# Kernel optimization log

Hardware: AMD Instinct MI355X
Metric: run time of the kernel (lower is better)

Reference implementation:

```python
import jax, jax.numpy as jnp
import numpy as np

N_NODES = 500_000
N_EDGES = 4_000_000


def setup_inputs() -> dict:
    key = jax.random.key(0)
    k1, k2, k3, k4 = jax.random.split(key, 4)
    x = jax.random.normal(k1, (N_NODES, 3), dtype=jnp.float32)
    edge_index = jax.random.randint(k2, (2, N_EDGES), 0, N_NODES, dtype=jnp.int32)
    # GCNConv(3, 16) and GCNConv(16, 1): weight [in, out], bias [out]
    W1 = jax.random.normal(k3, (3, 16), dtype=jnp.float32) / np.sqrt(3.0)
    b1 = jnp.zeros((16,), dtype=jnp.float32)
    W2 = jax.random.normal(k4, (16, 1), dtype=jnp.float32) / np.sqrt(16.0)
    b2 = jnp.zeros((1,), dtype=jnp.float32)
    return {"x": x, "edge_index": edge_index, "W1": W1, "b1": b1, "W2": W2, "b2": b2}


def gcn_conv(x, edge_index, W, b):
    """PyG GCNConv: add self-loops, symmetric deg^-1/2 normalization,
    linear transform, scatter-add aggregation to target nodes, bias."""
    n = x.shape[0]
    loop = jnp.arange(n, dtype=edge_index.dtype)
    row = jnp.concatenate([edge_index[0], loop])  # source nodes
    col = jnp.concatenate([edge_index[1], loop])  # target nodes
    deg = jax.ops.segment_sum(jnp.ones_like(col, dtype=x.dtype), col, num_segments=n)
    deg_inv_sqrt = jnp.where(deg > 0, jax.lax.rsqrt(jnp.maximum(deg, 1.0)), 0.0)
    norm = deg_inv_sqrt[row] * deg_inv_sqrt[col]  # [E+N]
    h = x @ W  # [N, out]
    msg = h[row] * norm[:, None]  # gather + scale, [E+N, out]
    out = jax.ops.segment_sum(msg, col, num_segments=n)  # scatter-add
    return out + b


def reference(x, edge_index, W1, b1, W2, b2):
    h = jax.nn.relu(gcn_conv(x, edge_index, W1, b1))
    return gcn_conv(h, edge_index, W2, b2)  # [N, 1]
```

## Files before the change

kernel.cpp:

```cpp
#include <hip/hip_runtime.h>
#include <hip/hip_fp16.h>


typedef float vf4 __attribute__((ext_vector_type(4)));

#define NB 512
#define SHIFT 10
#define SLICE 1024
#define CAP 11264
#define P1T 1024
#define P1PER 16
#define P1G 256
#define SENT 0xFFFFFFFFu

__global__ __launch_bounds__(1024) void p1_partition(
        const int* __restrict__ row, const int* __restrict__ col,
        unsigned* __restrict__ gcur, unsigned* __restrict__ buf, int E) {
    __shared__ unsigned hist[NB];
    __shared__ unsigned loff[NB], lcur[NB], gbase[NB];
    __shared__ unsigned stage[P1T * P1PER];
    __shared__ unsigned wsum[16];
    int t = threadIdx.x;
    if (t < NB) hist[t] = 0;
    __syncthreads();
    int per = (E + P1G - 1) / P1G;
    per = (per + 3) & ~3;
    long long base = (long long)blockIdx.x * per;
    long long eend = base + per; if (eend > E) eend = E;
    int nch = (per + 4095) / 4096;
    unsigned ent[P1PER];
    int bkt[P1PER];
#pragma unroll
    for (int ch = 0; ch < 4; ch++) {
        if (ch < nch) {
            long long e = base + (long long)ch * 4096 + 4 * t;
            if (e + 3 < eend) {
                int4 c4 = *(const int4*)(col + e);
                int4 r4 = *(const int4*)(row + e);
                int cs[4] = {c4.x, c4.y, c4.z, c4.w};
                int rs[4] = {r4.x, r4.y, r4.z, r4.w};
#pragma unroll
                for (int u = 0; u < 4; u++) {
                    int j = ch * 4 + u;
                    ent[j] = ((unsigned)rs[u] << SHIFT) | (unsigned)(cs[u] & (SLICE - 1));
                    bkt[j] = cs[u] >> SHIFT;
                    atomicAdd(&hist[bkt[j]], 1u);
                }
            } else {
#pragma unroll
                for (int u = 0; u < 4; u++) {
                    int j = ch * 4 + u;
                    long long ee = e + u;
                    if (ee < eend) {
                        int c = col[ee], r = row[ee];
                        ent[j] = ((unsigned)r << SHIFT) | (unsigned)(c & (SLICE - 1));
                        bkt[j] = c >> SHIFT;
                        atomicAdd(&hist[bkt[j]], 1u);
                    } else bkt[j] = -1;
                }
            }
        } else {
#pragma unroll
            for (int u = 0; u < 4; u++) bkt[ch * 4 + u] = -1;
        }
    }
    __syncthreads();
    unsigned myc = 0, v = 0;
    int lane = t & 63, w = t >> 6;
    if (t < NB) {
        myc = hist[t];
        v = myc;
#pragma unroll
        for (int d = 1; d < 64; d <<= 1) {
            unsigned o = __shfl_up(v, d, 64);
            if (lane >= d) v += o;
        }
        if (lane == 63) wsum[w] = v;
    }
    __syncthreads();
    if (w == 0) {
        unsigned s = (lane < 8) ? wsum[lane] : 0u, sv = s;
#pragma unroll
        for (int d = 1; d < 8; d <<= 1) {
            unsigned o = __shfl_up(sv, d, 64);
            if (lane >= d) sv += o;
        }
        if (lane < 8) wsum[lane] = sv - s;
    }
    __syncthreads();
    if (t < NB) {
        unsigned excl = v - myc + wsum[w];
        loff[t] = excl;
        lcur[t] = excl;
        unsigned padded = (myc + 15u) & ~15u;
        gbase[t] = padded ? atomicAdd(&gcur[t], padded) : 0u;
        hist[t] = padded;
    }
    __syncthreads();
#pragma unroll
    for (int j = 0; j < P1PER; j++) {
        if (bkt[j] >= 0) {
            unsigned p = atomicAdd(&lcur[bkt[j]], 1u);
            stage[p] = ent[j];
        }
    }
    __syncthreads();
    if (t < NB) {
        unsigned c = myc, padded = hist[t], lo = loff[t], gb = gbase[t];
        unsigned* dst = buf + (size_t)t * CAP + gb;
        for (unsigned s = 0; s + 4 <= padded && gb + s + 4 <= CAP; s += 4) {
            uint4 q;
            q.x = (s + 0 < c) ? stage[lo + s + 0] : SENT;
            q.y = (s + 1 < c) ? stage[lo + s + 1] : SENT;
            q.z = (s + 2 < c) ? stage[lo + s + 2] : SENT;
            q.w = (s + 3 < c) ? stage[lo + s + 3] : SENT;
            *(uint4*)(dst + s) = q;
        }
    }
}

__global__ __launch_bounds__(1024) void k2a1(
        const unsigned* __restrict__ gcur, const unsigned* __restrict__ buf,
        const float* __restrict__ x, uint2* __restrict__ xs4h,
        unsigned* __restrict__ pstart, int N) {
    __shared__ unsigned cnts[SLICE];
    __shared__ unsigned wsum[16];
    int b = blockIdx.x, t = threadIdx.x;
    cnts[t] = 0;
    __syncthreads();
    unsigned ext = min(gcur[b], (unsigned)CAP);
    const unsigned* bp = buf + (size_t)b * CAP;
    for (unsigned i = 4 * t; i < ext; i += 4096) {
        uint4 q = *(const uint4*)(bp + i);
        if (q.x != SENT) atomicAdd(&cnts[q.x & (SLICE - 1)], 1u);
        if (q.y != SENT) atomicAdd(&cnts[q.y & (SLICE - 1)], 1u);
        if (q.z != SENT) atomicAdd(&cnts[q.z & (SLICE - 1)], 1u);
        if (q.w != SENT) atomicAdd(&cnts[q.w & (SLICE - 1)], 1u);
    }
    __syncthreads();
    unsigned myc = cnts[t];
    unsigned pc = (myc + 3u) & ~3u;
    unsigned v = pc;
    int lane = t & 63, w = t >> 6;
#pragma unroll
    for (int d = 1; d < 64; d <<= 1) {
        unsigned o = __shfl_up(v, d, 64);
        if (lane >= d) v += o;
    }
    if (lane == 63) wsum[w] = v;
    __syncthreads();
    if (w == 0) {
        unsigned s = (lane < 16) ? wsum[lane] : 0u, sv = s;
#pragma unroll
        for (int d = 1; d < 16; d <<= 1) {
            unsigned o = __shfl_up(sv, d, 64);
            if (lane >= d) sv += o;
        }
        if (lane < 16) wsum[lane] = sv - s;
    }
    __syncthreads();
    unsigned excl = v - pc + wsum[w];
    int c = (b << SHIFT) + t;
    pstart[c] = (excl << 8) | min(myc, 255u);
    if (c < N) {
        float d = rsqrtf(1.0f + (float)myc);
        __half2 h01 = __floats2half2_rn(d * x[3 * c], d * x[3 * c + 1]);
        __half2 h23 = __floats2half2_rn(d * x[3 * c + 2], 0.f);
        uint2 u;
        u.x = *(unsigned*)&h01;
        u.y = *(unsigned*)&h23;
        xs4h[c] = u;
    }
}

__global__ __launch_bounds__(1024) void k2bf(
        const unsigned* __restrict__ gcur, const unsigned* __restrict__ buf,
        const unsigned* __restrict__ pstart, const uint2* __restrict__ xs4h,
        const float* __restrict__ W1, const float* __restrict__ b1,
        const float* __restrict__ W2, unsigned* __restrict__ buf2,
        float* __restrict__ hs2, int N) {
    __shared__ __align__(16) unsigned sorted[CAP];
    __shared__ unsigned pos[SLICE];
    __shared__ unsigned stot;
    __shared__ float sW[48], sb[16], sw2[16];
    int b = blockIdx.x, t = threadIdx.x;
    if (t < 48) sW[t] = W1[t];
    if (t < 16) { sb[t] = b1[t]; sw2[t] = W2[t]; }
    unsigned meta = pstart[(b << SHIFT) + t];
    pos[t] = meta >> 8;
    if (t == SLICE - 1) {
        unsigned tt = (meta >> 8) + (((meta & 255u) + 3u) & ~3u);
        stot = min(tt, (unsigned)CAP);
    }
    __syncthreads();
    unsigned ext = min(gcur[b], (unsigned)CAP);
    const unsigned* bp = buf + (size_t)b * CAP;
    for (unsigned i = 4 * t; i < ext; i += 4096) {
        uint4 q = *(const uint4*)(bp + i);
        if (q.x != SENT) { unsigned p = atomicAdd(&pos[q.x & (SLICE - 1)], 1u); if (p < CAP) sorted[p] = q.x >> SHIFT; }
        if (q.y != SENT) { unsigned p = atomicAdd(&pos[q.y & (SLICE - 1)], 1u); if (p < CAP) sorted[p] = q.y >> SHIFT; }
        if (q.z != SENT) { unsigned p = atomicAdd(&pos[q.z & (SLICE - 1)], 1u); if (p < CAP) sorted[p] = q.z >> SHIFT; }
        if (q.w != SENT) { unsigned p = atomicAdd(&pos[q.w & (SLICE - 1)], 1u); if (p < CAP) sorted[p] = q.w >> SHIFT; }
    }
    __syncthreads();
    unsigned tot = stot;
    unsigned* b2p = buf2 + (size_t)b * CAP;
    for (unsigned i = 4 * t; i < tot; i += 4096)
        *(uint4*)(b2p + i) = *(const uint4*)(sorted + i);
    int c = (b << SHIFT) + t;
    if (c >= N) return;
    unsigned cnt = meta & 255u;
    unsigned base = meta >> 8;
    float d = rsqrtf(1.0f + (float)cnt);
    uint2 us = xs4h[c];
    float2 fs = __half22float2(*(__half2*)&us.x);
    float a0 = fs.x, a1 = fs.y, a2 = __low2float(*(__half2*)&us.y);
    unsigned j = 0;
    for (; j + 4 <= cnt; j += 4) {
        uint4 rr = *(const uint4*)(sorted + base + j);
        uint2 u0 = xs4h[rr.x], u1 = xs4h[rr.y], u2 = xs4h[rr.z], u3 = xs4h[rr.w];
        float2 f0 = __half22float2(*(__half2*)&u0.x); float g0 = __low2float(*(__half2*)&u0.y);
        float2 f1 = __half22float2(*(__half2*)&u1.x); float g1 = __low2float(*(__half2*)&u1.y);
        float2 f2 = __half22float2(*(__half2*)&u2.x); float g2 = __low2float(*(__half2*)&u2.y);
        float2 f3 = __half22float2(*(__half2*)&u3.x); float g3 = __low2float(*(__half2*)&u3.y);
        a0 += (f0.x + f1.x) + (f2.x + f3.x);
        a1 += (f0.y + f1.y) + (f2.y + f3.y);
        a2 += (g0 + g1) + (g2 + g3);
    }
    for (; j < cnt; j++) {
        uint2 u = xs4h[sorted[base + j]];
        float2 f = __half22float2(*(__half2*)&u.x);
        a0 += f.x; a1 += f.y; a2 += __low2float(*(__half2*)&u.y);
    }
    float s = 0.f;
#pragma unroll
    for (int k = 0; k < 16; k++) {
        float z = fmaxf(d * (a0 * sW[k] + a1 * sW[16 + k] + a2 * sW[32 + k]) + sb[k], 0.f);
        s += z * sw2[k];
    }
    hs2[c] = d * s;
}

__global__ __launch_bounds__(1024) void k2c(
        const unsigned* __restrict__ pstart, const unsigned* __restrict__ buf2,
        const float* __restrict__ hs2, const float* __restrict__ b2,
        float* __restrict__ out, int N) {
    int b = blockIdx.x, t = threadIdx.x;
    int c = (b << SHIFT) + t;
    if (c >= N) return;
    unsigned meta = pstart[c];
    const unsigned* sp = buf2 + (size_t)b * CAP + (meta >> 8);
    unsigned cnt = meta & 255u;
    float d = rsqrtf(1.0f + (float)cnt);
    float s = hs2[c];
    unsigned j = 0;
    for (; j + 4 <= cnt; j += 4) {
        uint4 rr = *(const uint4*)(sp + j);
        float v0 = hs2[rr.x], v1 = hs2[rr.y], v2 = hs2[rr.z], v3 = hs2[rr.w];
        s += (v0 + v1) + (v2 + v3);
    }
    for (; j < cnt; j++) s += hs2[sp[j]];
    out[c] = d * s + b2[0];
}

__global__ void fb_deg(const int* __restrict__ col, float* __restrict__ deg, int E) {
    int e = blockIdx.x * blockDim.x + threadIdx.x;
    if (e < E) atomicAdd(&deg[col[e]], 1.0f);
}
__global__ void fb_pass_a(const float* __restrict__ x, const float* __restrict__ deg,
                          float* __restrict__ dis, vf4* __restrict__ xs4, int N) {
    int i = blockIdx.x * blockDim.x + threadIdx.x;
    if (i >= N) return;
    float d = rsqrtf(deg[i] + 1.0f);
    dis[i] = d;
    vf4 v; v.x = d * x[3 * i]; v.y = d * x[3 * i + 1]; v.z = d * x[3 * i + 2]; v.w = 0.f;
    xs4[i] = v;
}
__global__ void fb_aggx(const int* __restrict__ ei, const float* __restrict__ xs4,
                        float* __restrict__ accx, int E) {
    int t = blockIdx.x * blockDim.x + threadIdx.x;
    int e = t >> 2, k = t & 3;
    if (e >= E) return;
    int r = ei[e], c = ei[E + e];
    float val = xs4[4 * r + k];
    if (k < 3) atomicAdd(&accx[4 * c + k], val);
}
__global__ void fb_post1(const vf4* __restrict__ accx, const vf4* __restrict__ xs4,
                         const float* __restrict__ dis, const float* __restrict__ W1,
                         const float* __restrict__ b1, const float* __restrict__ W2,
                         float* __restrict__ hs2, int N) {
    __shared__ float sW[48], sb[16], sw2[16];
    if (threadIdx.x < 48) sW[threadIdx.x] = W1[threadIdx.x];
    if (threadIdx.x < 16) { sb[threadIdx.x] = b1[threadIdx.x]; sw2[threadIdx.x] = W2[threadIdx.x]; }
    __syncthreads();
    int i = blockIdx.x * blockDim.x + threadIdx.x;
    if (i >= N) return;
    vf4 a = accx[i], self = xs4[i];
    float a0 = a.x + self.x, a1 = a.y + self.y, a2 = a.z + self.z;
    float d = dis[i], s = 0.f;
#pragma unroll
    for (int k = 0; k < 16; k++) {
        float z = fmaxf(d * (a0 * sW[k] + a1 * sW[16 + k] + a2 * sW[32 + k]) + sb[k], 0.f);
        s += z * sw2[k];
    }
    hs2[i] = d * s;
}
__global__ void fb_agg2(const int* __restrict__ ei, const float* __restrict__ hs2,
                        float* __restrict__ acc2, int E) {
    int e = blockIdx.x * blockDim.x + threadIdx.x;
    if (e >= E) return;
    atomicAdd(&acc2[ei[E + e]], hs2[ei[e]]);
}
__global__ void fb_fin(const float* __restrict__ acc2, const float* __restrict__ hs2,
                       const float* __restrict__ dis, const float* __restrict__ b2,
                       float* __restrict__ out, int N) {
    int i = blockIdx.x * blockDim.x + threadIdx.x;
    if (i < N) out[i] = dis[i] * (acc2[i] + hs2[i]) + b2[0];
}

extern "C" void kernel_launch(void* const* d_in, const int* in_sizes, int n_in,
                              void* d_out, int out_size, void* d_ws, size_t ws_size,
                              hipStream_t stream) {
    const float* x  = (const float*)d_in[0];
    const int*   ei = (const int*)d_in[1];
    const float* W1 = (const float*)d_in[2];
    const float* b1 = (const float*)d_in[3];
    const float* W2 = (const float*)d_in[4];
    const float* b2 = (const float*)d_in[5];
    float* out = (float*)d_out;

    const int N = in_sizes[0] / 3;
    const int E = in_sizes[1] / 2;
    const int* row = ei;
    const int* col = ei + E;

    float* ws = (float*)d_ws;
    size_t need = (size_t)(1024 + 2 * (size_t)NB * CAP + 3 * (size_t)N
                           + (size_t)NB * SLICE) * 4;

    if (ws_size >= need) {
        unsigned* gcur = (unsigned*)ws;
        unsigned* buf  = (unsigned*)ws + 1024;
        unsigned* buf2 = buf + (size_t)NB * CAP;
        uint2* xs4h = (uint2*)(buf2 + (size_t)NB * CAP);
        float* hs2  = (float*)(xs4h + N);
        unsigned* pstart = (unsigned*)(hs2 + N);

        hipMemsetAsync(gcur, 0, 1024 * sizeof(unsigned), stream);
        p1_partition<<<P1G, P1T, 0, stream>>>(row, col, gcur, buf, E);
        k2a1<<<NB, 1024, 0, stream>>>(gcur, buf, x, xs4h, pstart, N);
        k2bf<<<NB, 1024, 0, stream>>>(gcur, buf, pstart, xs4h, W1, b1, W2, buf2, hs2, N);
        k2c<<<NB, 1024, 0, stream>>>(pstart, buf2, hs2, b2, out, N);
    } else {
        float* deg = ws;
        float* dis = ws + (size_t)N;
        vf4*  xs4 = (vf4*)(ws + 2 * (size_t)N);
        float* accx = ws + 6 * (size_t)N;
        float* hs2 = ws + 10 * (size_t)N;
        float* acc2 = ws + 11 * (size_t)N;
        const int B = 256;
        hipMemsetAsync(deg, 0, (size_t)N * sizeof(float), stream);
        hipMemsetAsync(accx, 0, 4 * (size_t)N * sizeof(float), stream);
        hipMemsetAsync(acc2, 0, (size_t)N * sizeof(float), stream);
        fb_deg<<<(E + B - 1) / B, B, 0, stream>>>(col, deg, E);
        fb_pass_a<<<(N + B - 1) / B, B, 0, stream>>>(x, deg, dis, xs4, N);
        long long t4 = (long long)E * 4;
        fb_aggx<<<(int)((t4 + B - 1) / B), B, 0, stream>>>(ei, (const float*)xs4, accx, E);
        fb_post1<<<(N + B - 1) / B, B, 0, stream>>>((const vf4*)accx, xs4, dis, W1, b1, W2, hs2, N);
        fb_agg2<<<(E + B - 1) / B, B, 0, stream>>>(ei, hs2, acc2, E);
        fb_fin<<<(N + B - 1) / B, B, 0, stream>>>(acc2, hs2, dis, b2, out, N);
    }
}
```

Baseline: 157.4 us.

## Reduce bucket padding, use wave-cooperative bucket writes, unroll k2c gather by eight

The partition kernel now pads each per-block bucket chunk to a multiple of 4 instead of 16 entries. This shrinks the sentinel-filled gaps that later kernels must read and skip. The bucket flush changes from one thread writing 16-byte vectors per bucket to a whole wave writing 32 buckets with coalesced scalar stores across lanes, which spreads the work more evenly. It also adds an occupancy hint to three kernels and an 8-wide unrolled gather loop in k2c to keep more loads in flight. The risks are more register pressure and narrower stores.

```diff
diff --git a/kernel.cpp b/kernel.cpp
--- a/kernel.cpp
+++ b/kernel.cpp
@@ -17,7 +17,7 @@
         const int* __restrict__ row, const int* __restrict__ col,
         unsigned* __restrict__ gcur, unsigned* __restrict__ buf, int E) {
     __shared__ unsigned hist[NB];
-    __shared__ unsigned loff[NB], lcur[NB], gbase[NB];
+    __shared__ unsigned loff[NB], lcur[NB], gbase[NB], bcnt[NB];
     __shared__ unsigned stage[P1T * P1PER];
     __shared__ unsigned wsum[16];
     int t = threadIdx.x;
@@ -92,7 +92,8 @@
         unsigned excl = v - myc + wsum[w];
         loff[t] = excl;
         lcur[t] = excl;
-        unsigned padded = (myc + 15u) & ~15u;
+        bcnt[t] = myc;
+        unsigned padded = (myc + 3u) & ~3u;
         gbase[t] = padded ? atomicAdd(&gcur[t], padded) : 0u;
         hist[t] = padded;
     }
@@ -105,21 +106,19 @@
         }
     }
     __syncthreads();
-    if (t < NB) {
-        unsigned c = myc, padded = hist[t], lo = loff[t], gb = gbase[t];
-        unsigned* dst = buf + (size_t)t * CAP + gb;
-        for (unsigned s = 0; s + 4 <= padded && gb + s + 4 <= CAP; s += 4) {
-            uint4 q;
-            q.x = (s + 0 < c) ? stage[lo + s + 0] : SENT;
-            q.y = (s + 1 < c) ? stage[lo + s + 1] : SENT;
-            q.z = (s + 2 < c) ? stage[lo + s + 2] : SENT;
-            q.w = (s + 3 < c) ? stage[lo + s + 3] : SENT;
-            *(uint4*)(dst + s) = q;
-        }
-    }
-}
-
-__global__ __launch_bounds__(1024) void k2a1(
+    for (int bb = 0; bb < 32; bb++) {
+        int bk = (w << 5) + bb;
+        unsigned c = bcnt[bk], padded = hist[bk];
+        unsigned lo = loff[bk], gb = gbase[bk];
+        unsigned* dst = buf + (size_t)bk * CAP + gb;
+        for (unsigned s = lane; s < padded; s += 64) {
+            unsigned val = (s < c) ? stage[lo + s] : SENT;
+            if (gb + s < CAP) dst[s] = val;
+        }
+    }
+}
+
+__global__ __launch_bounds__(1024, 8) void k2a1(
         const unsigned* __restrict__ gcur, const unsigned* __restrict__ buf,
         const float* __restrict__ x, uint2* __restrict__ xs4h,
         unsigned* __restrict__ pstart, int N) {
@@ -173,7 +172,7 @@
     }
 }
 
-__global__ __launch_bounds__(1024) void k2bf(
+__global__ __launch_bounds__(1024, 8) void k2bf(
         const unsigned* __restrict__ gcur, const unsigned* __restrict__ buf,
         const unsigned* __restrict__ pstart, const uint2* __restrict__ xs4h,
         const float* __restrict__ W1, const float* __restrict__ b1,
@@ -241,7 +240,7 @@
     hs2[c] = d * s;
 }
 
-__global__ __launch_bounds__(1024) void k2c(
+__global__ __launch_bounds__(1024, 8) void k2c(
         const unsigned* __restrict__ pstart, const unsigned* __restrict__ buf2,
         const float* __restrict__ hs2, const float* __restrict__ b2,
         float* __restrict__ out, int N) {
@@ -254,6 +253,13 @@
     float d = rsqrtf(1.0f + (float)cnt);
     float s = hs2[c];
     unsigned j = 0;
+    for (; j + 8 <= cnt; j += 8) {
+        uint4 ra = *(const uint4*)(sp + j);
+        uint4 rb = *(const uint4*)(sp + j + 4);
+        float v0 = hs2[ra.x], v1 = hs2[ra.y], v2 = hs2[ra.z], v3 = hs2[ra.w];
+        float v4 = hs2[rb.x], v5 = hs2[rb.y], v6 = hs2[rb.z], v7 = hs2[rb.w];
+        s += ((v0 + v1) + (v2 + v3)) + ((v4 + v5) + (v6 + v7));
+    }
     for (; j + 4 <= cnt; j += 4) {
         uint4 rr = *(const uint4*)(sp + j);
         float v0 = hs2[rr.x], v1 = hs2[rr.y], v2 = hs2[rr.z], v3 = hs2[rr.w];
```

Measured after the change: 157.5 us, median of 2. About the same (+0.1%).
